# Optimization experiments

Hardware: AMD Instinct MI355X
Metric: run time of the kernel (lower is better)

Reference implementation:

```python
import jax, jax.numpy as jnp
import numpy as np

B, T, E, QKV, H = 2, 2048, 1024, 1024, 16
DH = QKV // H
R_LAYER = 2

def rmsnorm(x):
    eps = jnp.finfo(x.dtype).eps
    return x * jax.lax.rsqrt(jnp.mean(x * x, axis=-1, keepdims=True) + eps)

def w_norm(w, n):
    # scale whole matrix so its (unbiased) std matches n**-0.5
    std = jnp.std(w, ddof=1)
    return w * (n ** -0.5 / (std + 1e-8))

def rotary(x, cos, sin):
    d = x.shape[-1] // 2
    x1, x2 = x[..., :d], x[..., d:]
    return jnp.concatenate([x1 * cos + x2 * sin, -x1 * sin + x2 * cos], axis=-1)

def w_split(w):
    w_qkv = w[:3 * QKV]                               # (3*QKV, E)
    w_sw = w[3 * QKV:5 * QKV].reshape(2 * E, QKV)     # (2*E, QKV)
    w_out = w[5 * QKV:]                               # (E, E)
    return w_qkv, w_sw, w_out

def aft(x, w_qkv):
    qkv = rmsnorm(x) @ w_qkv.T                        # (B,T,3*QKV)
    q, k, v = jnp.split(qkv, 3, axis=-1)
    q, k = rmsnorm(q), rmsnorm(k)
    wexp = jnp.exp(k)
    kv_c = jnp.cumsum(wexp * v, axis=1)
    w_c = jnp.cumsum(wexp, axis=1)
    y = jax.nn.sigmoid(q) * kv_c / (w_c + 1e-6)
    return x, y

def tea(x, cos, sin, w_qkv):
    qkv = (rmsnorm(x) @ w_qkv.T).reshape(B, T, H, 3 * DH)
    q, k, v = jnp.split(qkv, 3, axis=-1)              # each (B,T,H,DH)
    q, k = rotary(q, cos, sin), rotary(k, cos, sin)
    q, k = rmsnorm(q), rmsnorm(k)
    q = q.transpose(0, 2, 1, 3)                       # (B,H,T,DH)
    k = k.transpose(0, 2, 1, 3)
    v = v.transpose(0, 2, 1, 3)
    scores = jnp.einsum('bhqd,bhkd->bhqk', q, k) * DH ** -0.5
    mask = jnp.tril(jnp.ones((T, T), dtype=bool))
    scores = jnp.where(mask, scores, -jnp.inf)
    att = jax.nn.softmax(scores, axis=-1)
    y = jnp.einsum('bhqk,bhkd->bhqd', att, v)
    return x, y.transpose(0, 2, 1, 3).reshape(B, T, QKV)

def swiglu(x, y, w_sw, w_out, ret_oa=True):
    uv = y @ w_sw.T                                   # (B,T,2*E)
    u, v = jnp.split(uv, 2, axis=-1)
    out = x + (u * jax.nn.silu(v)) @ w_out.T
    if not ret_oa:
        return out
    o = rmsnorm(u.reshape(B * T, -1))
    a = v.reshape(B * T, -1)
    oa = jax.nn.softmax((o.T @ a) * E ** -0.5, axis=-1)  # (E,E)
    return out, oa

def setup_inputs():
    key = jax.random.key(0)
    k1, k2 = jax.random.split(key)
    x = jax.random.normal(k1, (B, T, E), dtype=jnp.float32)
    s = 3 ** 0.5 * E ** -0.5
    w = jax.random.uniform(k2, (5 * QKV + E, E), dtype=jnp.float32, minval=-s, maxval=s)
    half = DH // 2
    inv_freq = 1.0 / (10000.0 ** (jnp.arange(half, dtype=jnp.float32) / half))
    freqs = jnp.outer(jnp.arange(T, dtype=jnp.float32), inv_freq)  # (T, half)
    cos = jnp.cos(freqs)[:, None, :]                  # (T,1,half) broadcasts over (B,T,H,half)
    sin = jnp.sin(freqs)[:, None, :]
    return {"x": x, "w": w, "cos": cos, "sin": sin}

def reference(x, w, cos, sin):
    for i in range(R_LAYER):
        w_qkv, w_sw, w_out = w_split(w)
        w_qkv = w_norm(w_qkv, E)
        w_sw = w_norm(w_sw, QKV)
        w_out = w_norm(w_out, E)
        if (i + 1) % 4 == 0:
            x, y = tea(x, cos, sin, w_qkv)
        else:
            x, y = aft(x, w_qkv)
        x, oa = swiglu(x, y, w_sw, w_out, ret_oa=True)
        # RetentionMechanism.forward: hypernetwork weight mixing
        wT = w_norm(w @ oa, 5 * QKV + E)
        w = wT * jax.nn.silu(w) + w
    w_qkv, w_sw, w_out = w_split(w)                   # note: no w_norm on final split (matches source)
    x, y = tea(x, cos, sin, w_qkv)
    return swiglu(x, y, w_sw, w_out, ret_oa=False)
```

## Files before the change

### kernel.cpp

```cpp
#include <hip/hip_runtime.h>
#include <hip/hip_bf16.h>
#include <math.h>

#define TPB 256

constexpr int Bc = 2, Tc = 2048, Ec = 1024, QKVc = 1024, Hc = 16, DHc = 64;
constexpr long BT = (long)Bc * Tc;
constexpr int WR = 5 * QKVc + Ec;
constexpr float F32_EPS = 1.1920928955078125e-07f;
constexpr int NCH = 64, CHL = Tc / NCH;

typedef __attribute__((ext_vector_type(8))) short short8;
typedef __attribute__((ext_vector_type(4))) float f32x4;

__device__ __forceinline__ unsigned short f2bu(float f) {
    union { __hip_bfloat16 h; unsigned short u; } c; c.h = __float2bfloat16(f); return c.u;
}
__device__ __forceinline__ float bu2f(unsigned short u) {
    union { __hip_bfloat16 h; unsigned short u; } c; c.u = u; return __bfloat162float(c.h);
}
__device__ __forceinline__ float ldval(const float* p) { return *p; }
__device__ __forceinline__ float ldval(const unsigned short* p) { return bu2f(*p); }

__device__ __forceinline__ void gload_lds16(const void* g, void* l) {
    __builtin_amdgcn_global_load_lds((const __attribute__((address_space(1))) void*)g,
                                     (__attribute__((address_space(3))) void*)l, 16, 0, 0);
}

template<int CTRL>
__device__ __forceinline__ float dppf(float x) {
    union { float f; int i; } a, b;
    a.f = x;
    b.i = __builtin_amdgcn_update_dpp(0, a.i, CTRL, 0xF, 0xF, true);
    return b.f;
}
__device__ __forceinline__ float max16(float v) {
    v = fmaxf(v, dppf<0xB1>(v));
    v = fmaxf(v, dppf<0x4E>(v));
    v = fmaxf(v, dppf<0x124>(v));
    v = fmaxf(v, dppf<0x128>(v));
    return v;
}
__device__ __forceinline__ float sum16(float v) {
    v += dppf<0xB1>(v);
    v += dppf<0x4E>(v);
    v += dppf<0x124>(v);
    v += dppf<0x128>(v);
    return v;
}

__global__ void k_std_partial3(const float* __restrict__ w, float* __restrict__ out) {
    __shared__ float ls[TPB], lss[TPB];
    int seg = blockIdx.y;
    long base = (seg == 0) ? 0L : (seg == 1 ? 3072L * 1024 : 5120L * 1024);
    long n    = (seg == 0) ? 3072L * 1024 : (seg == 1 ? 2048L * 1024 : 1024L * 1024);
    const float* p = w + base;
    float s = 0.f, ss = 0.f;
    for (long i = (long)blockIdx.x * TPB + threadIdx.x; i < n; i += 256L * TPB) {
        float v = p[i]; s += v; ss += v * v;
    }
    ls[threadIdx.x] = s; lss[threadIdx.x] = ss; __syncthreads();
    for (int o = 128; o > 0; o >>= 1) {
        if (threadIdx.x < o) { ls[threadIdx.x] += ls[threadIdx.x + o]; lss[threadIdx.x] += lss[threadIdx.x + o]; }
        __syncthreads();
    }
    if (threadIdx.x == 0) { out[seg * 512 + blockIdx.x] = ls[0]; out[seg * 512 + 256 + blockIdx.x] = lss[0]; }
}

__global__ void k_std_final3(const float* __restrict__ part, float* __restrict__ scales) {
    __shared__ float ls[TPB], lss[TPB];
    for (int seg = 0; seg < 3; ++seg) {
        ls[threadIdx.x] = part[seg * 512 + threadIdx.x];
        lss[threadIdx.x] = part[seg * 512 + 256 + threadIdx.x];
        __syncthreads();
        for (int o = 128; o > 0; o >>= 1) {
            if (threadIdx.x < o) { ls[threadIdx.x] += ls[threadIdx.x + o]; lss[threadIdx.x] += lss[threadIdx.x + o]; }
            __syncthreads();
        }
        if (threadIdx.x == 0) {
            float n = (seg == 0) ? 3145728.0f : (seg == 1 ? 2097152.0f : 1048576.0f);
            float var = (lss[0] - ls[0] * ls[0] / n) / (n - 1.0f);
            scales[seg] = 0.03125f / (sqrtf(fmaxf(var, 0.0f)) + 1e-8f);
        }
        __syncthreads();
    }
}

__global__ void k_std_finalB(const float* __restrict__ red, float n, float rs, float* __restrict__ scale) {
    __shared__ float ls[TPB], lss[TPB];
    float s = 0.f, ss = 0.f;
    for (int i = threadIdx.x; i < 6144; i += TPB) { s += red[i]; ss += red[8192 + i]; }
    ls[threadIdx.x] = s; lss[threadIdx.x] = ss; __syncthreads();
    for (int o = 128; o > 0; o >>= 1) {
        if (threadIdx.x < o) { ls[threadIdx.x] += ls[threadIdx.x + o]; lss[threadIdx.x] += lss[threadIdx.x + o]; }
        __syncthreads();
    }
    if (threadIdx.x == 0) {
        float var = (lss[0] - ls[0] * ls[0] / n) / (n - 1.0f);
        scale[0] = rs / (sqrtf(fmaxf(var, 0.0f)) + 1e-8f);
    }
}

__global__ void k_rms_qk(unsigned short* __restrict__ qkv) {
    __shared__ float red[TPB];
    int bid = blockIdx.x;
    long row = bid >> 1; int half = bid & 1;
    unsigned short* p = qkv + row * 3072 + half * 1024;
    ushort4 v = *(const ushort4*)(p + threadIdx.x * 4);
    float f0 = bu2f(v.x), f1 = bu2f(v.y), f2 = bu2f(v.z), f3 = bu2f(v.w);
    red[threadIdx.x] = f0 * f0 + f1 * f1 + f2 * f2 + f3 * f3;
    __syncthreads();
    for (int o = 128; o > 0; o >>= 1) {
        if (threadIdx.x < o) red[threadIdx.x] += red[threadIdx.x + o];
        __syncthreads();
    }
    float sc = rsqrtf(red[0] / 1024.0f + F32_EPS);
    ushort4 o4; o4.x = f2bu(f0 * sc); o4.y = f2bu(f1 * sc); o4.z = f2bu(f2 * sc); o4.w = f2bu(f3 * sc);
    *(ushort4*)(p + threadIdx.x * 4) = o4;
}

__global__ void k_rms1024b(const float* __restrict__ in, unsigned short* __restrict__ out, long ldin, long ldout) {
    __shared__ float red[TPB];
    long row = blockIdx.x;
    float4 v = *(const float4*)(in + row * ldin + threadIdx.x * 4);
    float ss = v.x * v.x + v.y * v.y + v.z * v.z + v.w * v.w;
    red[threadIdx.x] = ss; __syncthreads();
    for (int o = 128; o > 0; o >>= 1) {
        if (threadIdx.x < o) red[threadIdx.x] += red[threadIdx.x + o];
        __syncthreads();
    }
    float sc = rsqrtf(red[0] / 1024.0f + F32_EPS);
    ushort4 o4; o4.x = f2bu(v.x * sc); o4.y = f2bu(v.y * sc); o4.z = f2bu(v.z * sc); o4.w = f2bu(v.w * sc);
    *(ushort4*)(out + row * ldout + threadIdx.x * 4) = o4;
}

__global__ void k_cast_bf16(const float* __restrict__ in, unsigned short* __restrict__ out, long n4) {
    long i = (long)blockIdx.x * TPB + threadIdx.x;
    if (i >= n4) return;
    float4 v = *(const float4*)(in + i * 4);
    ushort4 o; o.x = f2bu(v.x); o.y = f2bu(v.y); o.z = f2bu(v.z); o.w = f2bu(v.w);
    *(ushort4*)(out + i * 4) = o;
}

__global__ void k_merge2(const unsigned short* __restrict__ p0, const unsigned short* __restrict__ p1,
                         const float* __restrict__ resid, float* __restrict__ outp, long n4) {
    long i = (long)blockIdx.x * TPB + threadIdx.x;
    if (i >= n4) return;
    ushort4 a = *(const ushort4*)(p0 + i * 4);
    ushort4 b = *(const ushort4*)(p1 + i * 4);
    float4 o;
    o.x = bu2f(a.x) + bu2f(b.x); o.y = bu2f(a.y) + bu2f(b.y);
    o.z = bu2f(a.z) + bu2f(b.z); o.w = bu2f(a.w) + bu2f(b.w);
    if (resid) {
        float4 r = *(const float4*)(resid + i * 4);
        o.x += r.x; o.y += r.y; o.z += r.z; o.w += r.w;
    }
    *(float4*)(outp + i * 4) = o;
}

__global__ void k_merge2rms(const unsigned short* __restrict__ p0, const unsigned short* __restrict__ p1,
                            const float* __restrict__ resid, float* __restrict__ xout,
                            unsigned short* __restrict__ xbn) {
    __shared__ float red[TPB];
    long row = blockIdx.x;
    long i = row * 256 + threadIdx.x;
    ushort4 a = *(const ushort4*)(p0 + i * 4);
    ushort4 b = *(const ushort4*)(p1 + i * 4);
    float4 r = *(const float4*)(resid + i * 4);
    float4 o;
    o.x = bu2f(a.x) + bu2f(b.x) + r.x; o.y = bu2f(a.y) + bu2f(b.y) + r.y;
    o.z = bu2f(a.z) + bu2f(b.z) + r.z; o.w = bu2f(a.w) + bu2f(b.w) + r.w;
    *(float4*)(xout + i * 4) = o;
    red[threadIdx.x] = o.x * o.x + o.y * o.y + o.z * o.z + o.w * o.w;
    __syncthreads();
    for (int off = 128; off > 0; off >>= 1) {
        if (threadIdx.x < off) red[threadIdx.x] += red[threadIdx.x + off];
        __syncthreads();
    }
    float sc = rsqrtf(red[0] / 1024.0f + F32_EPS);
    ushort4 ob; ob.x = f2bu(o.x * sc); ob.y = f2bu(o.y * sc); ob.z = f2bu(o.z * sc); ob.w = f2bu(o.w * sc);
    *(ushort4*)(xbn + i * 4) = ob;
}

__global__ void k_merge2stat(const unsigned short* __restrict__ p0, const unsigned short* __restrict__ p1,
                             float* __restrict__ outp, float* __restrict__ red) {
    __shared__ float ls[TPB], lss[TPB];
    long i = (long)blockIdx.x * TPB + threadIdx.x;
    ushort4 a = *(const ushort4*)(p0 + i * 4);
    ushort4 b = *(const ushort4*)(p1 + i * 4);
    float4 o;
    o.x = bu2f(a.x) + bu2f(b.x); o.y = bu2f(a.y) + bu2f(b.y);
    o.z = bu2f(a.z) + bu2f(b.z); o.w = bu2f(a.w) + bu2f(b.w);
    *(float4*)(outp + i * 4) = o;
    ls[threadIdx.x] = o.x + o.y + o.z + o.w;
    lss[threadIdx.x] = o.x * o.x + o.y * o.y + o.z * o.z + o.w * o.w;
    __syncthreads();
    for (int off = 128; off > 0; off >>= 1) {
        if (threadIdx.x < off) { ls[threadIdx.x] += ls[threadIdx.x + off]; lss[threadIdx.x] += lss[threadIdx.x + off]; }
        __syncthreads();
    }
    if (threadIdx.x == 0) { red[blockIdx.x] = ls[0]; red[8192 + blockIdx.x] = lss[0]; }
}

template<typename TI>
__global__ void k_tcast(const TI* __restrict__ in, long ldi, long sIn,
                        unsigned short* __restrict__ out, long ldo, long sOut,
                        const float* __restrict__ rowscale) {
    __shared__ float tile[64][65];
    const TI* ip = in + (long)blockIdx.z * sIn;
    unsigned short* op = out + (long)blockIdx.z * sOut;
    int r0 = blockIdx.y * 64, c0 = blockIdx.x * 64;
    int tid = threadIdx.x;
    int rr = tid >> 4, cc = (tid & 15) * 4;
    #pragma unroll
    for (int u = 0; u < 4; ++u) {
        int r = rr + u * 16;
        float sc = rowscale ? rowscale[r0 + r] : 1.0f;
        #pragma unroll
        for (int j = 0; j < 4; ++j)
            tile[r][cc + j] = ldval(ip + (long)(r0 + r) * ldi + c0 + cc + j) * sc;
    }
    __syncthreads();
    #pragma unroll
    for (int u = 0; u < 4; ++u) {
        int c = rr + u * 16;
        ushort4 o;
        o.x = f2bu(tile[cc + 0][c]); o.y = f2bu(tile[cc + 1][c]);
        o.z = f2bu(tile[cc + 2][c]); o.w = f2bu(tile[cc + 3][c]);
        *(ushort4*)(op + (long)(c0 + c) * ldo + r0 + cc) = o;
    }
}

__global__ void k_tcast2(const unsigned short* __restrict__ uv, const float* __restrict__ uscale,
                         unsigned short* __restrict__ t1, unsigned short* __restrict__ t2) {
    __shared__ float tile[64][65];
    int z = blockIdx.z;
    const unsigned short* ip = uv + (z ? 1024 : 0);
    unsigned short* op = z ? t2 : t1;
    int r0 = blockIdx.y * 64, c0 = blockIdx.x * 64;
    int tid = threadIdx.x;
    int rr = tid >> 4, cc = (tid & 15) * 4;
    #pragma unroll
    for (int u = 0; u < 4; ++u) {
        int r = rr + u * 16;
        float sc = z ? 1.0f : uscale[r0 + r];
        ushort4 v = *(const ushort4*)(ip + (long)(r0 + r) * 2048 + c0 + cc);
        tile[r][cc + 0] = bu2f(v.x) * sc; tile[r][cc + 1] = bu2f(v.y) * sc;
        tile[r][cc + 2] = bu2f(v.z) * sc; tile[r][cc + 3] = bu2f(v.w) * sc;
    }
    __syncthreads();
    #pragma unroll
    for (int u = 0; u < 4; ++u) {
        int c = rr + u * 16;
        ushort4 o;
        o.x = f2bu(tile[cc + 0][c]); o.y = f2bu(tile[cc + 1][c]);
        o.z = f2bu(tile[cc + 2][c]); o.w = f2bu(tile[cc + 3][c]);
        *(ushort4*)(op + (long)(c0 + c) * 4096 + r0 + cc) = o;
    }
}

template<int WRITE_BF16>
__global__ __launch_bounds__(256)
void k_bgemm(int K,
             const unsigned short* __restrict__ A, int lda, long sA,
             const unsigned short* __restrict__ B, int ldb, long sB,
             void* __restrict__ C, int ldc, long sCi, long sSplit, int nsplit,
             const float* __restrict__ scale_ptr, float fscale,
             const float* __restrict__ addp, int ldadd) {
    __shared__ unsigned short Asl[128 * 64];
    __shared__ unsigned short Bsl[128 * 64];
    int bz = blockIdx.z;
    int batch = bz, sp = 0;
    if (nsplit > 1) { batch = bz / nsplit; sp = bz - batch * nsplit; }
    int m0 = blockIdx.y * 128, n0 = blockIdx.x * 128;
    const unsigned short* Ap = A + (long)batch * sA + (long)sp * K;
    const unsigned short* Bp = B + (long)batch * sB + (long)sp * K;
    int tid = threadIdx.x, lane = tid & 63, wave = tid >> 6;
    int wr = wave >> 1, wc = wave & 1;
    f32x4 acc[4][4] = {};
    for (int k0 = 0; k0 < K; k0 += 64) {
        #pragma unroll
        for (int cc = 0; cc < 4; ++cc) {
            int bu = (wave * 4 + cc) * 64;
            int uidx = bu + lane;
            int r = uidx >> 3, slot = uidx & 7;
            int gu = slot ^ (r & 7);
            gload_lds16(Ap + (long)(m0 + r) * lda + k0 + gu * 8, Asl + bu * 8);
        }
        #pragma unroll
        for (int cc = 0; cc < 4; ++cc) {
            int bu = (wave * 4 + cc) * 64;
            int uidx = bu + lane;
            int r = uidx >> 3, slot = uidx & 7;
            int gu = slot ^ (r & 7);
            gload_lds16(Bp + (long)(n0 + r) * ldb + k0 + gu * 8, Bsl + bu * 8);
        }
        __syncthreads();
        #pragma unroll
        for (int ksub = 0; ksub < 2; ++ksub) {
            short8 av[4], bv[4];
            #pragma unroll
            for (int m = 0; m < 4; ++m) {
                int r = wr * 64 + m * 16 + (lane & 15);
                int slot = (ksub * 4 + (lane >> 4)) ^ (r & 7);
                av[m] = *(const short8*)(Asl + r * 64 + slot * 8);
            }
            #pragma unroll
            for (int n = 0; n < 4; ++n) {
                int r = wc * 64 + n * 16 + (lane & 15);
                int slot = (ksub * 4 + (lane >> 4)) ^ (r & 7);
                bv[n] = *(const short8*)(Bsl + r * 64 + slot * 8);
            }
            #pragma unroll
            for (int m = 0; m < 4; ++m)
                #pragma unroll
                for (int n = 0; n < 4; ++n)
                    acc[m][n] = __builtin_amdgcn_mfma_f32_16x16x32_bf16(av[m], bv[n], acc[m][n], 0, 0, 0);
        }
        __syncthreads();
    }
    float s = fscale * (scale_ptr ? scale_ptr[0] : 1.0f);
    long cbase = (long)batch * sCi + (long)sp * sSplit;
    int row0 = m0 + wr * 64, col0 = n0 + wc * 64 + (lane & 15);
    int rbase = (lane >> 4) * 4;
    #pragma unroll
    for (int m = 0; m < 4; ++m)
        #pragma unroll
        for (int i = 0; i < 4; ++i) {
            long row = row0 + m * 16 + rbase + i;
            #pragma unroll
            for (int n = 0; n < 4; ++n) {
                long col = col0 + n * 16;
                float v = acc[m][n][i] * s;
                if (addp) v += addp[row * (long)ldadd + col];
                long idx = cbase + row * ldc + col;
                if (WRITE_BF16) ((unsigned short*)C)[idx] = f2bu(v);
                else ((float*)C)[idx] = v;
            }
        }
}

__global__ __launch_bounds__(256)
void k_flash_split(const unsigned short* __restrict__ hq, const unsigned short* __restrict__ hk,
                   const unsigned short* __restrict__ hvT,
                   unsigned short* __restrict__ opart, float* __restrict__ mpart, float* __restrict__ lpart) {
    __shared__ unsigned short P_lds[4][32 * 72];
    int lane = threadIdx.x & 63, wave = threadIdx.x >> 6;
    unsigned short* P = P_lds[wave];
    int g = lane >> 4, c = lane & 15;
    unsigned bid = blockIdx.x;
    unsigned bswz = (bid & 7) * 160 + (bid >> 3);
    unsigned gi = bswz * 4 + wave;
    unsigned bh = gi / 160, itr = gi % 160;
    int item = 159 - (int)itr;
    int strip, chunk;
    if (item < 16)      { strip = item;                 chunk = 0; }
    else if (item < 48) { strip = 16 + (item - 16) / 2; chunk = (item - 16) & 1; }
    else if (item < 96) { strip = 32 + (item - 48) / 3; chunk = (item - 48) % 3; }
    else                { strip = 48 + (item - 96) / 4; chunk = (item - 96) & 3; }
    int q0 = strip * 32;
    int nt = (q0 + 32 + 63) >> 6;
    int ti0 = chunk * 8;
    int ti1 = ti0 + 8 < nt ? ti0 + 8 : nt;
    const unsigned short* qb = hq + (long)bh * Tc * 64;
    const unsigned short* kb = hk + (long)bh * Tc * 64;
    const unsigned short* vtb = hvT + (long)bh * 64 * Tc;

    short8 qf[2][2];
    #pragma unroll
    for (int mf = 0; mf < 2; ++mf)
        #pragma unroll
        for (int ks = 0; ks < 2; ++ks)
            qf[mf][ks] = *(const short8*)(qb + (long)(q0 + mf * 16 + c) * 64 + ks * 32 + g * 8);

    f32x4 o_acc[2][4] = {};
    float m_run[2][4], lpp[2][4];
    #pragma unroll
    for (int mf = 0; mf < 2; ++mf)
        #pragma unroll
        for (int i = 0; i < 4; ++i) { m_run[mf][i] = -3.0e38f; lpp[mf][i] = 0.f; }

    for (int ti = ti0; ti < ti1; ++ti) {
        int kt = ti * 64;
        short8 vf[2][4];
        #pragma unroll
        for (int ks = 0; ks < 2; ++ks)
            #pragma unroll
            for (int df = 0; df < 4; ++df)
                vf[ks][df] = *(const short8*)(vtb + (long)(df * 16 + c) * Tc + kt + ks * 32 + g * 8);
        f32x4 s_acc[2][4] = {};
        #pragma unroll
        for (int ks = 0; ks < 2; ++ks) {
            short8 kf[4];
            #pragma unroll
            for (int nf = 0; nf < 4; ++nf)
                kf[nf] = *(const short8*)(kb + (long)(kt + nf * 16 + c) * 64 + ks * 32 + g * 8);
            #pragma unroll
            for (int mf = 0; mf < 2; ++mf)
                #pragma unroll
                for (int nf = 0; nf < 4; ++nf)
                    s_acc[mf][nf] = __builtin_amdgcn_mfma_f32_16x16x32_bf16(qf[mf][ks], kf[nf], s_acc[mf][nf], 0, 0, 0);
        }
        if (ti == nt - 1) {
            #pragma unroll
            for (int mf = 0; mf < 2; ++mf)
                #pragma unroll
                for (int nf = 0; nf < 4; ++nf)
                    #pragma unroll
                    for (int i = 0; i < 4; ++i)
                        if ((kt + nf * 16 + c) > (q0 + mf * 16 + g * 4 + i)) s_acc[mf][nf][i] = -1.0e30f;
        }
        float pm[2][4];
        #pragma unroll
        for (int mf = 0; mf < 2; ++mf)
            #pragma unroll
            for (int i = 0; i < 4; ++i)
                pm[mf][i] = max16(fmaxf(fmaxf(s_acc[mf][0][i], s_acc[mf][1][i]),
                                        fmaxf(s_acc[mf][2][i], s_acc[mf][3][i])));
        float mg = 0.f;
        #pragma unroll
        for (int mf = 0; mf < 2; ++mf)
            #pragma unroll
            for (int i = 0; i < 4; ++i) {
                pm[mf][i] *= 0.125f;
                mg = fmaxf(mg, pm[mf][i] - m_run[mf][i]);
            }
        if (__any(mg > 8.0f)) {
            #pragma unroll
            for (int mf = 0; mf < 2; ++mf)
                #pragma unroll
                for (int i = 0; i < 4; ++i) {
                    float mn = fmaxf(m_run[mf][i], pm[mf][i]);
                    float corr = __expf(m_run[mf][i] - mn);
                    m_run[mf][i] = mn;
                    lpp[mf][i] *= corr;
                    #pragma unroll
                    for (int df = 0; df < 4; ++df) o_acc[mf][df][i] *= corr;
                }
        }
        #pragma unroll
        for (int mf = 0; mf < 2; ++mf)
            #pragma unroll
            for (int nf = 0; nf < 4; ++nf)
                #pragma unroll
                for (int i = 0; i < 4; ++i) {
                    float p = __expf(fmaf(s_acc[mf][nf][i], 0.125f, -m_run[mf][i]));
                    P[(mf * 16 + g * 4 + i) * 72 + nf * 16 + c] = f2bu(p);
                    lpp[mf][i] += p;
                }
        #pragma unroll
        for (int ks = 0; ks < 2; ++ks) {
            short8 pa[2];
            #pragma unroll
            for (int mf = 0; mf < 2; ++mf)
                pa[mf] = *(const short8*)(P + (mf * 16 + c) * 72 + ks * 32 + g * 8);
            #pragma unroll
            for (int mf = 0; mf < 2; ++mf)
                #pragma unroll
                for (int df = 0; df < 4; ++df)
                    o_acc[mf][df] = __builtin_amdgcn_mfma_f32_16x16x32_bf16(pa[mf], vf[ks][df], o_acc[mf][df], 0, 0, 0);
        }
    }
    #pragma unroll
    for (int mf = 0; mf < 2; ++mf)
        #pragma unroll
        for (int i = 0; i < 4; ++i)
            lpp[mf][i] = sum16(lpp[mf][i]);
    long pbase = (long)(bh * 160 + item);
    #pragma unroll
    for (int mf = 0; mf < 2; ++mf)
        #pragma unroll
        for (int i = 0; i < 4; ++i) {
            int row_l = mf * 16 + g * 4 + i;
            #pragma unroll
            for (int df = 0; df < 4; ++df)
                opart[pbase * 2048 + row_l * 64 + df * 16 + c] = f2bu(o_acc[mf][df][i]);
            if (c == 0) {
                mpart[pbase * 32 + row_l] = m_run[mf][i];
                lpart[pbase * 32 + row_l] = lpp[mf][i];
            }
        }
}

__global__ __launch_bounds__(256)
void k_flash_merge(const unsigned short* __restrict__ opart, const float* __restrict__ mpart,
                   const float* __restrict__ lpart, unsigned short* __restrict__ yout) {
    int bs = blockIdx.x;
    int bh = bs >> 6, strip = bs & 63;
    int b = bh >> 4, h = bh & 15;
    int np, base;
    if (strip < 16)      { np = 1; base = strip; }
    else if (strip < 32) { np = 2; base = 16 + (strip - 16) * 2; }
    else if (strip < 48) { np = 3; base = 48 + (strip - 32) * 3; }
    else                 { np = 4; base = 96 + (strip - 48) * 4; }
    long p0 = (long)(bh * 160 + base);
    int tid = threadIdx.x;
    int r = tid >> 3, c0 = (tid & 7) * 8;
    float M = -3.0e38f;
    for (int p = 0; p < np; ++p) M = fmaxf(M, mpart[(p0 + p) * 32 + r]);
    float L = 0.f;
    float acc[8] = {};
    for (int p = 0; p < np; ++p) {
        float sc = __expf(mpart[(p0 + p) * 32 + r] - M);
        L += lpart[(p0 + p) * 32 + r] * sc;
        const unsigned short* op = opart + (p0 + p) * 2048 + r * 64 + c0;
        ushort4 a = *(const ushort4*)op;
        ushort4 bq = *(const ushort4*)(op + 4);
        acc[0] += bu2f(a.x) * sc; acc[1] += bu2f(a.y) * sc;
        acc[2] += bu2f(a.z) * sc; acc[3] += bu2f(a.w) * sc;
        acc[4] += bu2f(bq.x) * sc; acc[5] += bu2f(bq.y) * sc;
        acc[6] += bu2f(bq.z) * sc; acc[7] += bu2f(bq.w) * sc;
    }
    float inv = 1.0f / L;
    long row = (long)b * Tc + strip * 32 + r;
    unsigned short* yp = yout + row * 1024 + h * 64 + c0;
    ushort4 o1, o2;
    o1.x = f2bu(acc[0] * inv); o1.y = f2bu(acc[1] * inv); o1.z = f2bu(acc[2] * inv); o1.w = f2bu(acc[3] * inv);
    o2.x = f2bu(acc[4] * inv); o2.y = f2bu(acc[5] * inv); o2.z = f2bu(acc[6] * inv); o2.w = f2bu(acc[7] * inv);
    *(ushort4*)yp = o1;
    *(ushort4*)(yp + 4) = o2;
}

__global__ void k_aft_p1(const unsigned short* __restrict__ qkv, float* __restrict__ cw, float* __restrict__ cs) {
    int id = blockIdx.x * TPB + threadIdx.x;
    int bc = id & 2047, ch = id >> 11;
    int b = bc >> 10, c = bc & 1023;
    const unsigned short* base = qkv + ((long)(b * Tc + ch * CHL)) * 3072 + c;
    float sw = 0.f, sv = 0.f;
    for (int i = 0; i < CHL; ++i) {
        float k = bu2f(base[1024]), v = bu2f(base[2048]);
        float e = __expf(k);
        sw += e; sv += e * v;
        base += 3072;
    }
    cw[ch * 2048 + bc] = sw; cs[ch * 2048 + bc] = sv;
}

__global__ void k_aft_p2(float* __restrict__ cw, float* __restrict__ cs) {
    int bc = blockIdx.x * TPB + threadIdx.x;
    float rw = 0.f, rv = 0.f;
    for (int ch = 0; ch < NCH; ++ch) {
        long idx = (long)ch * 2048 + bc;
        float tw = cw[idx], tv = cs[idx];
        cw[idx] = rw; cs[idx] = rv; rw += tw; rv += tv;
    }
}

__global__ void k_aft_p3(const unsigned short* __restrict__ qkv, const float* __restrict__ cw,
                         const float* __restrict__ cs, unsigned short* __restrict__ y) {
    int id = blockIdx.x * TPB + threadIdx.x;
    int bc = id & 2047, ch = id >> 11;
    int b = bc >> 10, c = bc & 1023;
    float aw = cw[ch * 2048 + bc], av = cs[ch * 2048 + bc];
    long t0 = (long)b * Tc + ch * CHL;
    const unsigned short* base = qkv + t0 * 3072 + c;
    unsigned short* yp = y + t0 * 1024 + c;
    for (int i = 0; i < CHL; ++i) {
        float q = bu2f(base[0]), k = bu2f(base[1024]), v = bu2f(base[2048]);
        float e = __expf(k);
        av += e * v; aw += e;
        float sig = 1.0f / (1.0f + __expf(-q));
        yp[0] = f2bu(sig * av / (aw + 1e-6f));
        base += 3072; yp += 1024;
    }
}

__global__ void k_silu_rms(const unsigned short* __restrict__ uv, unsigned short* __restrict__ g,
                           float* __restrict__ rs) {
    __shared__ float red[TPB];
    long row = blockIdx.x;
    const unsigned short* up = uv + row * 2048;
    ushort4 u4 = *(const ushort4*)(up + threadIdx.x * 4);
    ushort4 v4 = *(const ushort4*)(up + 1024 + threadIdx.x * 4);
    float u0 = bu2f(u4.x), u1 = bu2f(u4.y), u2 = bu2f(u4.z), u3 = bu2f(u4.w);
    float v0 = bu2f(v4.x), v1 = bu2f(v4.y), v2 = bu2f(v4.z), v3 = bu2f(v4.w);
    ushort4 o;
    o.x = f2bu(u0 * v0 / (1.f + __expf(-v0)));
    o.y = f2bu(u1 * v1 / (1.f + __expf(-v1)));
    o.z = f2bu(u2 * v2 / (1.f + __expf(-v2)));
    o.w = f2bu(u3 * v3 / (1.f + __expf(-v3)));
    *(ushort4*)(g + row * 1024 + threadIdx.x * 4) = o;
    red[threadIdx.x] = u0 * u0 + u1 * u1 + u2 * u2 + u3 * u3;
    __syncthreads();
    for (int off = 128; off > 0; off >>= 1) {
        if (threadIdx.x < off) red[threadIdx.x] += red[threadIdx.x + off];
        __syncthreads();
    }
    if (threadIdx.x == 0) rs[row] = rsqrtf(red[0] / 1024.0f + F32_EPS);
}

__global__ void k_silu_gate(const unsigned short* __restrict__ uv, unsigned short* __restrict__ g, long n4) {
    long i = (long)blockIdx.x * TPB + threadIdx.x;
    if (i >= n4) return;
    long r = i >> 8, c4 = i & 255;
    ushort4 u4 = *(const ushort4*)(uv + r * 2048 + c4 * 4);
    ushort4 v4 = *(const ushort4*)(uv + r * 2048 + 1024 + c4 * 4);
    float u0 = bu2f(u4.x), u1 = bu2f(u4.y), u2 = bu2f(u4.z), u3 = bu2f(u4.w);
    float v0 = bu2f(v4.x), v1 = bu2f(v4.y), v2 = bu2f(v4.z), v3 = bu2f(v4.w);
    ushort4 o;
    o.x = f2bu(u0 * v0 / (1.f + __expf(-v0)));
    o.y = f2bu(u1 * v1 / (1.f + __expf(-v1)));
    o.z = f2bu(u2 * v2 / (1.f + __expf(-v2)));
    o.w = f2bu(u3 * v3 / (1.f + __expf(-v3)));
    *(ushort4*)(g + r * 1024 + c4 * 4) = o;
}

__global__ void k_wupdate(float* __restrict__ wout, const float* __restrict__ win,
                          const float* __restrict__ p, const float* __restrict__ scale,
                          unsigned short* __restrict__ wb, long n4) {
    long i = (long)blockIdx.x * TPB + threadIdx.x;
    if (i >= n4) return;
    float s = scale[0];
    float4 wv = *(const float4*)(win + i * 4);
    float4 pv = *(const float4*)(p + i * 4);
    float4 o;
    o.x = pv.x * s * (wv.x / (1.f + __expf(-wv.x))) + wv.x;
    o.y = pv.y * s * (wv.y / (1.f + __expf(-wv.y))) + wv.y;
    o.z = pv.z * s * (wv.z / (1.f + __expf(-wv.z))) + wv.z;
    o.w = pv.w * s * (wv.w / (1.f + __expf(-wv.w))) + wv.w;
    *(float4*)(wout + i * 4) = o;
    ushort4 ob; ob.x = f2bu(o.x); ob.y = f2bu(o.y); ob.z = f2bu(o.z); ob.w = f2bu(o.w);
    *(ushort4*)(wb + i * 4) = ob;
}

__global__ void k_softmax4(const float* __restrict__ parts, float* __restrict__ outb, float fscale) {
    __shared__ float red[TPB];
    __shared__ float rowbuf[1024];
    long row = blockIdx.x;
    const float* p0 = parts + row * 1024;
    for (int c = threadIdx.x; c < 1024; c += TPB) {
        float v = p0[c] + p0[c + 1048576] + p0[c + 2097152] + p0[c + 3145728];
        rowbuf[c] = v * fscale;
    }
    __syncthreads();
    float m = -3.0e38f;
    for (int c = threadIdx.x; c < 1024; c += TPB) m = fmaxf(m, rowbuf[c]);
    red[threadIdx.x] = m; __syncthreads();
    for (int o = 128; o > 0; o >>= 1) {
        if (threadIdx.x < o) red[threadIdx.x] = fmaxf(red[threadIdx.x], red[threadIdx.x + o]);
        __syncthreads();
    }
    m = red[0]; __syncthreads();
    float sum = 0.f;
    for (int c = threadIdx.x; c < 1024; c += TPB) sum += __expf(rowbuf[c] - m);
    red[threadIdx.x] = sum; __syncthreads();
    for (int o = 128; o > 0; o >>= 1) {
        if (threadIdx.x < o) red[threadIdx.x] += red[threadIdx.x + o];
        __syncthreads();
    }
    float inv = 1.0f / red[0];
    for (int c = threadIdx.x; c < 1024; c += TPB)
        outb[row * 1024 + c] = __expf(rowbuf[c] - m) * inv;
}

__global__ void k_rot_split(const unsigned short* __restrict__ qkvp, const float* __restrict__ cosp,
                            const float* __restrict__ sinp, unsigned short* __restrict__ hq,
                            unsigned short* __restrict__ hk, unsigned short* __restrict__ hv) {
    __shared__ float row[3072];
    __shared__ float cs[32], sn[32];
    int bt = blockIdx.x;
    int b = bt >> 11, t = bt & 2047;
    const unsigned short* src = qkvp + (long)bt * 3072;
    #pragma unroll
    for (int u = 0; u < 3; ++u) {
        int idx = threadIdx.x + u * 256;
        ushort4 v = *(const ushort4*)(src + idx * 4);
        row[idx * 4 + 0] = bu2f(v.x); row[idx * 4 + 1] = bu2f(v.y);
        row[idx * 4 + 2] = bu2f(v.z); row[idx * 4 + 3] = bu2f(v.w);
    }
    if (threadIdx.x < 32) { cs[threadIdx.x] = cosp[t * 32 + threadIdx.x]; sn[threadIdx.x] = sinp[t * 32 + threadIdx.x]; }
    __syncthreads();
    int h = threadIdx.x >> 4, li = threadIdx.x & 15;
    int base = h * 192;
    long obase = ((long)(b * Hc + h) * Tc + t) * 64 + li * 4;
    {
        float r[4]; float ss = 0.f;
        #pragma unroll
        for (int j = 0; j < 4; ++j) {
            int d = li * 4 + j;
            float val = (d < 32) ? (row[base + d] * cs[d] + row[base + d + 32] * sn[d])
                                 : (-row[base + d - 32] * sn[d - 32] + row[base + d] * cs[d - 32]);
            r[j] = val; ss += val * val;
        }
        ss = sum16(ss);
        float sc = rsqrtf(ss / 64.0f + F32_EPS);
        ushort4 o; o.x = f2bu(r[0] * sc); o.y = f2bu(r[1] * sc); o.z = f2bu(r[2] * sc); o.w = f2bu(r[3] * sc);
        *(ushort4*)(hq + obase) = o;
    }
    {
        int kb = base + 64;
        float r[4]; float ss = 0.f;
        #pragma unroll
        for (int j = 0; j < 4; ++j) {
            int d = li * 4 + j;
            float val = (d < 32) ? (row[kb + d] * cs[d] + row[kb + d + 32] * sn[d])
                                 : (-row[kb + d - 32] * sn[d - 32] + row[kb + d] * cs[d - 32]);
            r[j] = val; ss += val * val;
        }
        ss = sum16(ss);
        float sc = rsqrtf(ss / 64.0f + F32_EPS);
        ushort4 o; o.x = f2bu(r[0] * sc); o.y = f2bu(r[1] * sc); o.z = f2bu(r[2] * sc); o.w = f2bu(r[3] * sc);
        *(ushort4*)(hk + obase) = o;
    }
    {
        ushort4 o;
        o.x = f2bu(row[base + 128 + li * 4 + 0]); o.y = f2bu(row[base + 128 + li * 4 + 1]);
        o.z = f2bu(row[base + 128 + li * 4 + 2]); o.w = f2bu(row[base + 128 + li * 4 + 3]);
        *(ushort4*)(hv + obase) = o;
    }
}

extern "C" void kernel_launch(void* const* d_in, const int* in_sizes, int n_in,
                              void* d_out, int out_size, void* d_ws, size_t ws_size,
                              hipStream_t stream) {
    const float* x_in = (const float*)d_in[0];
    const float* w_in = (const float*)d_in[1];
    const float* cos_in = (const float*)d_in[2];
    const float* sin_in = (const float*)d_in[3];
    float* out = (float*)d_out;
    float* ws = (float*)d_ws;

    long off = 0;
    float* w_cur = ws + off;  off += (long)WR * Ec;
    float* w_tmp = ws + off;  off += (long)WR * Ec;
    float* xbuf  = ws + off;  off += BT * Ec;
    float* R     = ws + off;  off += BT * 3L * QKVc;
    float* oab   = ws + off;  off += (long)Ec * Ec;
    float* red   = ws + off;  off += 16384;
    float* scales= ws + off;  off += 16;
    float* uscale= ws + off;  off += 4096;
    float* chw   = ws + off;  off += 2048L * NCH;
    float* chs   = ws + off;  off += 2048L * NCH;
    unsigned short* qkvb  = (unsigned short*)R;
    unsigned short* uvb   = qkvb + 12582912L;
    unsigned short* opartb= qkvb;
    unsigned short* wsplit = qkvb;
    unsigned short* osplit = uvb;
    float* mpart = oab;
    float* lpart = oab + 5120L * 32;

    unsigned short* bp = (unsigned short*)(ws + off);
    long bo = 0;
    unsigned short* wb  = bp + bo; bo += (long)WR * Ec;
    unsigned short* xbn = bp + bo; bo += BT * Ec;
    unsigned short* ybn = bp + bo; bo += BT * Ec;
    unsigned short* gbn = bp + bo; bo += BT * Ec;
    unsigned short* t1  = bp + bo; bo += BT * Ec;
    unsigned short* t2  = bp + bo; bo += BT * Ec;
    unsigned short* t3  = bp + bo; bo += BT * Ec;
    unsigned short* t4  = bp + bo; bo += BT * Ec;

    const float rsWR = 1.0f / sqrtf(6144.0f);
    const long wsw = 3072L * 1024, wout = 5120L * 1024;

    k_cast_bf16<<<(int)(((long)WR * Ec / 4) / TPB), TPB, 0, stream>>>(w_in, wb, (long)WR * Ec / 4);
    k_rms1024b<<<BT, TPB, 0, stream>>>(x_in, xbn, 1024, 1024);

    for (int layer = 0; layer < 2; ++layer) {
        const float* wsrc = layer == 0 ? w_in : w_cur;
        const float* xsrc = layer == 0 ? x_in : xbuf;
        k_std_partial3<<<dim3(256, 3), TPB, 0, stream>>>(wsrc, red);
        k_std_final3<<<1, TPB, 0, stream>>>(red, scales);
        k_bgemm<1><<<dim3(24, 32, 1), TPB, 0, stream>>>(
            1024, xbn, 1024, 0, wb, 1024, 0, qkvb, 3072, 0, 0, 1, scales + 0, 1.0f, nullptr, 0);
        k_rms_qk<<<8192, TPB, 0, stream>>>(qkvb);
        k_aft_p1<<<(2048 * NCH) / TPB, TPB, 0, stream>>>(qkvb, chw, chs);
        k_aft_p2<<<2048 / TPB, TPB, 0, stream>>>(chw, chs);
        k_aft_p3<<<(2048 * NCH) / TPB, TPB, 0, stream>>>(qkvb, chw, chs, ybn);
        k_bgemm<1><<<dim3(16, 32, 1), TPB, 0, stream>>>(
            1024, ybn, 1024, 0, wb + wsw, 1024, 0, uvb, 2048, 0, 0, 1, scales + 1, 1.0f, nullptr, 0);
        k_silu_rms<<<BT, TPB, 0, stream>>>(uvb, gbn, uscale);
        k_tcast2<<<dim3(16, 64, 2), TPB, 0, stream>>>(uvb, uscale, t1, t2);
        k_bgemm<0><<<dim3(8, 8, 4), TPB, 0, stream>>>(
            1024, t1, 4096, 0, t2, 4096, 0, w_tmp, 1024, 0, 1048576L, 4, nullptr, 1.0f, nullptr, 0);
        k_softmax4<<<1024, TPB, 0, stream>>>(w_tmp, oab, 0.03125f);
        k_tcast<float><<<dim3(16, 16, 1), TPB, 0, stream>>>(oab, 1024, 0, t3, 1024, 0, nullptr);
        k_bgemm<1><<<dim3(8, 32, 2), TPB, 0, stream>>>(
            512, gbn, 1024, 0, wb + wout, 1024, 0, osplit, 1024, 0, 4194304L, 2, scales + 2, 1.0f, nullptr, 0);
        k_merge2rms<<<BT, TPB, 0, stream>>>(osplit, osplit + 4194304L, xsrc, xbuf, xbn);
        k_bgemm<1><<<dim3(8, 48, 2), TPB, 0, stream>>>(
            512, wb, 1024, 0, t3, 1024, 0, wsplit, 1024, 0, 6291456L, 2, nullptr, 1.0f, nullptr, 0);
        k_merge2stat<<<(int)(((long)WR * 1024 / 4) / TPB), TPB, 0, stream>>>(
            wsplit, wsplit + 6291456L, w_tmp, red);
        k_std_finalB<<<1, TPB, 0, stream>>>(red, (float)((long)WR * 1024), rsWR, scales + 3);
        k_wupdate<<<(int)(((long)WR * 1024 / 4) / TPB), TPB, 0, stream>>>(
            w_cur, wsrc, w_tmp, scales + 3, wb, (long)WR * 1024 / 4);
    }

    k_bgemm<1><<<dim3(24, 32, 1), TPB, 0, stream>>>(
        1024, xbn, 1024, 0, wb, 1024, 0, qkvb, 3072, 0, 0, 1, nullptr, 1.0f, nullptr, 0);
    k_rot_split<<<BT, TPB, 0, stream>>>(qkvb, cos_in, sin_in, t1, t2, t3);
    k_tcast<unsigned short><<<dim3(1, 32, 32), TPB, 0, stream>>>(
        t3, 64, (long)Tc * 64, t4, 2048, (long)Tc * 64, nullptr);
    k_flash_split<<<dim3(1280), TPB, 0, stream>>>(t1, t2, t4, opartb, mpart, lpart);
    k_flash_merge<<<dim3(2048), TPB, 0, stream>>>(opartb, mpart, lpart, ybn);
    k_bgemm<1><<<dim3(16, 32, 1), TPB, 0, stream>>>(
        1024, ybn, 1024, 0, wb + wsw, 1024, 0, uvb, 2048, 0, 0, 1, nullptr, 1.0f, nullptr, 0);
    k_silu_gate<<<(int)((BT * 1024 / 4) / TPB), TPB, 0, stream>>>(uvb, gbn, BT * 1024 / 4);
    k_bgemm<1><<<dim3(8, 32, 2), TPB, 0, stream>>>(
        512, gbn, 1024, 0, wb + wout, 1024, 0, qkvb, 1024, 0, 4194304L, 2, nullptr, 1.0f, nullptr, 0);
    k_merge2<<<(int)((BT * 1024 / 4) / TPB), TPB, 0, stream>>>(
        qkvb, qkvb + 4194304L, xbuf, out, BT * 1024 / 4);
}
```

Before: 734.4 us.

## Drop fp32 materialization of w@oa and split oa GEMM over eight K-slices

The statistics kernel no longer writes the merged fp32 w@oa product (about 25 MB per layer). It only reduces sum and sum-of-squares, and the weight-update kernel re-reads and sums the two bf16 split-K partials itself. Separately, the o^T@a GEMM now uses 8 K-splits of 512 instead of 4 of 1024, which puts more blocks on the GPU at the cost of doubling the partial buffer the softmax must sum. The partials go into the R region, and the softmax sums 8 slices instead of 4.

```diff
diff --git a/kernel.cpp b/kernel.cpp
--- a/kernel.cpp
+++ b/kernel.cpp
@@ -182,18 +182,16 @@
     *(ushort4*)(xbn + i * 4) = ob;
 }
 
-__global__ void k_merge2stat(const unsigned short* __restrict__ p0, const unsigned short* __restrict__ p1,
-                             float* __restrict__ outp, float* __restrict__ red) {
+__global__ void k_stat2(const unsigned short* __restrict__ p0, const unsigned short* __restrict__ p1,
+                        float* __restrict__ red) {
     __shared__ float ls[TPB], lss[TPB];
     long i = (long)blockIdx.x * TPB + threadIdx.x;
     ushort4 a = *(const ushort4*)(p0 + i * 4);
     ushort4 b = *(const ushort4*)(p1 + i * 4);
-    float4 o;
-    o.x = bu2f(a.x) + bu2f(b.x); o.y = bu2f(a.y) + bu2f(b.y);
-    o.z = bu2f(a.z) + bu2f(b.z); o.w = bu2f(a.w) + bu2f(b.w);
-    *(float4*)(outp + i * 4) = o;
-    ls[threadIdx.x] = o.x + o.y + o.z + o.w;
-    lss[threadIdx.x] = o.x * o.x + o.y * o.y + o.z * o.z + o.w * o.w;
+    float o0 = bu2f(a.x) + bu2f(b.x), o1 = bu2f(a.y) + bu2f(b.y);
+    float o2 = bu2f(a.z) + bu2f(b.z), o3 = bu2f(a.w) + bu2f(b.w);
+    ls[threadIdx.x] = o0 + o1 + o2 + o3;
+    lss[threadIdx.x] = o0 * o0 + o1 * o1 + o2 * o2 + o3 * o3;
     __syncthreads();
     for (int off = 128; off > 0; off >>= 1) {
         if (threadIdx.x < off) { ls[threadIdx.x] += ls[threadIdx.x + off]; lss[threadIdx.x] += lss[threadIdx.x + off]; }
@@ -606,30 +604,35 @@
 }
 
 __global__ void k_wupdate(float* __restrict__ wout, const float* __restrict__ win,
-                          const float* __restrict__ p, const float* __restrict__ scale,
-                          unsigned short* __restrict__ wb, long n4) {
+                          const unsigned short* __restrict__ p0, const unsigned short* __restrict__ p1,
+                          const float* __restrict__ scale, unsigned short* __restrict__ wb, long n4) {
     long i = (long)blockIdx.x * TPB + threadIdx.x;
     if (i >= n4) return;
     float s = scale[0];
     float4 wv = *(const float4*)(win + i * 4);
-    float4 pv = *(const float4*)(p + i * 4);
+    ushort4 a = *(const ushort4*)(p0 + i * 4);
+    ushort4 b = *(const ushort4*)(p1 + i * 4);
+    float p0f = bu2f(a.x) + bu2f(b.x), p1f = bu2f(a.y) + bu2f(b.y);
+    float p2f = bu2f(a.z) + bu2f(b.z), p3f = bu2f(a.w) + bu2f(b.w);
     float4 o;
-    o.x = pv.x * s * (wv.x / (1.f + __expf(-wv.x))) + wv.x;
-    o.y = pv.y * s * (wv.y / (1.f + __expf(-wv.y))) + wv.y;
-    o.z = pv.z * s * (wv.z / (1.f + __expf(-wv.z))) + wv.z;
-    o.w = pv.w * s * (wv.w / (1.f + __expf(-wv.w))) + wv.w;
+    o.x = p0f * s * (wv.x / (1.f + __expf(-wv.x))) + wv.x;
+    o.y = p1f * s * (wv.y / (1.f + __expf(-wv.y))) + wv.y;
+    o.z = p2f * s * (wv.z / (1.f + __expf(-wv.z))) + wv.z;
+    o.w = p3f * s * (wv.w / (1.f + __expf(-wv.w))) + wv.w;
     *(float4*)(wout + i * 4) = o;
     ushort4 ob; ob.x = f2bu(o.x); ob.y = f2bu(o.y); ob.z = f2bu(o.z); ob.w = f2bu(o.w);
     *(ushort4*)(wb + i * 4) = ob;
 }
 
-__global__ void k_softmax4(const float* __restrict__ parts, float* __restrict__ outb, float fscale) {
+__global__ void k_softmax8(const float* __restrict__ parts, float* __restrict__ outb, float fscale) {
     __shared__ float red[TPB];
     __shared__ float rowbuf[1024];
     long row = blockIdx.x;
     const float* p0 = parts + row * 1024;
     for (int c = threadIdx.x; c < 1024; c += TPB) {
-        float v = p0[c] + p0[c + 1048576] + p0[c + 2097152] + p0[c + 3145728];
+        float v = 0.f;
+        #pragma unroll
+        for (int sIdx = 0; sIdx < 8; ++sIdx) v += p0[c + (long)sIdx * 1048576];
         rowbuf[c] = v * fscale;
     }
     __syncthreads();
@@ -736,6 +739,7 @@
     unsigned short* opartb= qkvb;
     unsigned short* wsplit = qkvb;
     unsigned short* osplit = uvb;
+    float* oaparts = R;
     float* mpart = oab;
     float* lpart = oab + 5120L * 32;
 
@@ -771,20 +775,20 @@
             1024, ybn, 1024, 0, wb + wsw, 1024, 0, uvb, 2048, 0, 0, 1, scales + 1, 1.0f, nullptr, 0);
         k_silu_rms<<<BT, TPB, 0, stream>>>(uvb, gbn, uscale);
         k_tcast2<<<dim3(16, 64, 2), TPB, 0, stream>>>(uvb, uscale, t1, t2);
-        k_bgemm<0><<<dim3(8, 8, 4), TPB, 0, stream>>>(
-            1024, t1, 4096, 0, t2, 4096, 0, w_tmp, 1024, 0, 1048576L, 4, nullptr, 1.0f, nullptr, 0);
-        k_softmax4<<<1024, TPB, 0, stream>>>(w_tmp, oab, 0.03125f);
+        k_bgemm<0><<<dim3(8, 8, 8), TPB, 0, stream>>>(
+            512, t1, 4096, 0, t2, 4096, 0, oaparts, 1024, 0, 1048576L, 8, nullptr, 1.0f, nullptr, 0);
+        k_softmax8<<<1024, TPB, 0, stream>>>(oaparts, oab, 0.03125f);
         k_tcast<float><<<dim3(16, 16, 1), TPB, 0, stream>>>(oab, 1024, 0, t3, 1024, 0, nullptr);
         k_bgemm<1><<<dim3(8, 32, 2), TPB, 0, stream>>>(
             512, gbn, 1024, 0, wb + wout, 1024, 0, osplit, 1024, 0, 4194304L, 2, scales + 2, 1.0f, nullptr, 0);
         k_merge2rms<<<BT, TPB, 0, stream>>>(osplit, osplit + 4194304L, xsrc, xbuf, xbn);
         k_bgemm<1><<<dim3(8, 48, 2), TPB, 0, stream>>>(
             512, wb, 1024, 0, t3, 1024, 0, wsplit, 1024, 0, 6291456L, 2, nullptr, 1.0f, nullptr, 0);
-        k_merge2stat<<<(int)(((long)WR * 1024 / 4) / TPB), TPB, 0, stream>>>(
-            wsplit, wsplit + 6291456L, w_tmp, red);
+        k_stat2<<<(int)(((long)WR * 1024 / 4) / TPB), TPB, 0, stream>>>(
+            wsplit, wsplit + 6291456L, red);
         k_std_finalB<<<1, TPB, 0, stream>>>(red, (float)((long)WR * 1024), rsWR, scales + 3);
         k_wupdate<<<(int)(((long)WR * 1024 / 4) / TPB), TPB, 0, stream>>>(
-            w_cur, wsrc, w_tmp, scales + 3, wb, (long)WR * 1024 / 4);
+            w_cur, wsrc, wsplit, wsplit + 6291456L, scales + 3, wb, (long)WR * 1024 / 4);
     }
 
     k_bgemm<1><<<dim3(24, 32, 1), TPB, 0, stream>>>(
```

After: 712.9 us. -2.9%, faster.
